# Optimization experiments

Measured on AMD Instinct MI355X. Metric: run time of the kernel, lower is better.

Reference implementation:

```python
import jax, jax.numpy as jnp
import numpy as np
from jax import lax

DIM = 512
BATCH = 8
SEQ = 2048
LR = 0.1      # learning_rate (eta)
DECAY = 0.9   # decay_rate (lambda)


def setup_inputs() -> dict:
    key = jax.random.key(0)
    ks = jax.random.split(key, 5)
    scale = DIM ** -0.5
    return {
        "x": jax.random.normal(ks[0], (BATCH, SEQ, DIM), dtype=jnp.float32),
        "Wk": jax.random.normal(ks[1], (DIM, DIM), dtype=jnp.float32) * scale,
        "bk": jnp.zeros((DIM,), dtype=jnp.float32),
        "Wv": jax.random.normal(ks[2], (DIM, DIM), dtype=jnp.float32) * scale,
        "bv": jnp.zeros((DIM,), dtype=jnp.float32),
        "Wq": jax.random.normal(ks[3], (DIM, DIM), dtype=jnp.float32) * scale,
        "bq": jnp.zeros((DIM,), dtype=jnp.float32),
        "Wo": jax.random.normal(ks[4], (DIM, DIM), dtype=jnp.float32) * scale,
        "bo": jnp.zeros((DIM,), dtype=jnp.float32),
    }


def reference(x, Wk, bk, Wv, bv, Wq, bq, Wo, bo):
    B, S, D = x.shape
    # dense projections over all tokens at once
    k = x @ Wk + bk  # (B,S,D)
    v = x @ Wv + bv
    q = x @ Wq + bq

    state0 = jnp.zeros((B, D, D), dtype=x.dtype)

    def step(state, kvq):
        k_t, v_t, q_t = kvq                                  # each (B,D)
        mem = jnp.einsum('bd,bde->be', q_t, state)           # read BEFORE update
        new_state = DECAY * state + LR * jnp.einsum('bd,be->bde', k_t, v_t)
        return new_state, mem

    # scan over time: move seq axis to front
    kT = jnp.swapaxes(k, 0, 1)  # (S,B,D)
    vT = jnp.swapaxes(v, 0, 1)
    qT = jnp.swapaxes(q, 0, 1)
    final_state, mems = lax.scan(step, state0, (kT, vT, qT))  # mems (S,B,D)

    outputs = jnp.swapaxes(mems, 0, 1)                        # (B,S,D)
    out = outputs @ Wo + bo
    return out, final_state
```

## Files before the change

### kernel.cpp

```cpp
#include <hip/hip_runtime.h>
#include <math.h>


#define DIMD 512
#define SEQL 2048
#define LRC 0.1f
#define LAM64 1.1790184577738602e-3f
#define LAM128 1.3900845237714473e-6f
#define L2LAM -0.15200309344504997f

#define KVQ_ELEMS ((size_t)16384 * 512)
#define WSLAB ((size_t)512 * 512)

typedef __attribute__((ext_vector_type(8))) short bf16x8;
typedef __attribute__((ext_vector_type(4))) float f32x4;

__device__ __forceinline__ unsigned short f2bf(float f) {
  unsigned int u = __float_as_uint(f);
  u += 0x7FFFu + ((u >> 16) & 1u);
  return (unsigned short)(u >> 16);
}

__device__ __forceinline__ void gload16(const unsigned short* g, char* l) {
  __builtin_amdgcn_global_load_lds(
      (const __attribute__((address_space(1))) unsigned int*)g,
      (__attribute__((address_space(3))) unsigned int*)l, 16, 0, 0);
}

__global__ __launch_bounds__(256) void prep(
    const float* __restrict__ x, unsigned short* __restrict__ Abf,
    const float* __restrict__ Wq, const float* __restrict__ Wk,
    const float* __restrict__ Wv, const float* __restrict__ Wo,
    unsigned short* __restrict__ T) {
  const int blk = blockIdx.x;
  if (blk < 8192) {
    const size_t idx = ((size_t)blk * 256 + threadIdx.x) * 4;
    float4 v = *(const float4*)(x + idx);
    ushort4 u;
    u.x = f2bf(v.x); u.y = f2bf(v.y); u.z = f2bf(v.z); u.w = f2bf(v.w);
    *(ushort4*)(Abf + idx) = u;
    return;
  }
  const int r2 = blk - 8192;
  const int z = r2 >> 8;
  const int rem = r2 & 255;
  const int nb = (rem & 15) * 32, kb = (rem >> 4) * 32;
  const float* W = (z == 0) ? Wq : (z == 1) ? Wk : (z == 2) ? Wv : Wo;
  unsigned short* Tz = T + (size_t)z * WSLAB;
  __shared__ float tl[32][33];
  const int r = threadIdx.x >> 5, c = threadIdx.x & 31;
#pragma unroll
  for (int i = 0; i < 4; ++i)
    tl[r + i * 8][c] = W[(size_t)(kb + r + i * 8) * 512 + nb + c];
  __syncthreads();
#pragma unroll
  for (int i = 0; i < 4; ++i)
    Tz[(size_t)(nb + r + i * 8) * 512 + kb + c] = f2bf(tl[c][r + i * 8]);
}

template <int EMODE>
__global__ __launch_bounds__(256) void mfma_gemm(
    const unsigned short* __restrict__ A, int astr,
    const unsigned short* __restrict__ T0, const unsigned short* __restrict__ T1,
    const unsigned short* __restrict__ T2, int tstr,
    const float* __restrict__ b0, const float* __restrict__ b1,
    const float* __restrict__ b2,
    float* __restrict__ Cf,
    unsigned short* __restrict__ qh, unsigned short* __restrict__ kh,
    unsigned short* __restrict__ khT, unsigned short* __restrict__ vTp,
    int nkt) {
  const int z = blockIdx.z;
  const unsigned short* T = (z == 0) ? T0 : (z == 1) ? T1 : T2;
  const float* bias = (z == 0) ? b0 : (z == 1) ? b1 : b2;

  const int m0 = blockIdx.x * 128;
  const int n0 = blockIdx.y * 128;
  const int tid = threadIdx.x;
  const int lane = tid & 63;
  const int w = tid >> 6;
  const int wm = (w & 1) * 64;
  const int wn = (w >> 1) * 64;

  __shared__ __align__(16) char smem[EMODE == 0 ? 35840 : 32768];

  f32x4 acc[4][4];
  const f32x4 zf = {0.f, 0.f, 0.f, 0.f};
#pragma unroll
  for (int i = 0; i < 4; ++i)
#pragma unroll
    for (int j = 0; j < 4; ++j) acc[i][j] = zf;

  const int lr = lane >> 3;
  const int lo3 = lane & 7;
  const int xr = lo3 ^ lr;
  const int mbase = w * 32 + lr * 2 + (xr >> 2);
  const int kel = (xr & 3) * 8;
  const unsigned short* Ag = A + (size_t)(m0 + mbase) * astr + kel;
  const unsigned short* Tg = T + (size_t)(n0 + mbase) * tstr + kel;

#define ISSUE(KT, BUF)                                                     \
  {                                                                        \
    char* ab = smem + (BUF) * 8192 + w * 2048;                             \
    char* bb_ = smem + 16384 + (BUF) * 8192 + w * 2048;                    \
    _Pragma("unroll") for (int c = 0; c < 2; ++c) {                        \
      gload16(Ag + (size_t)(c * 16) * astr + (KT) * 32, ab + c * 1024);    \
      gload16(Tg + (size_t)(c * 16) * tstr + (KT) * 32, bb_ + c * 1024);   \
    }                                                                      \
  }

  const int fr = lane & 15;
  const int fg = lane >> 4;
  const int foff = ((((fr & 1) << 6) | (fg << 4)) ^ (((fr >> 1) & 7) << 4));
  const int aline = (wm >> 1) + (fr >> 1);
  const int bline = (wn >> 1) + (fr >> 1);

  ISSUE(0, 0);
  int bb = 0;
  for (int kt = 0; kt < nkt; ++kt) {
    if (kt + 1 < nkt) {
      ISSUE(kt + 1, bb ^ 1);
      asm volatile("s_waitcnt vmcnt(4)" ::: "memory");
    } else {
      asm volatile("s_waitcnt vmcnt(0)" ::: "memory");
    }
    __builtin_amdgcn_sched_barrier(0);
    __builtin_amdgcn_s_barrier();
    const char* pa = smem + bb * 8192 + aline * 128 + foff;
    const char* pb = smem + 16384 + bb * 8192 + bline * 128 + foff;
    bf16x8 af[4], bfr[4];
#pragma unroll
    for (int mi = 0; mi < 4; ++mi) af[mi] = *(const bf16x8*)(pa + mi * 1024);
#pragma unroll
    for (int ni = 0; ni < 4; ++ni) bfr[ni] = *(const bf16x8*)(pb + ni * 1024);
#pragma unroll
    for (int mi = 0; mi < 4; ++mi)
#pragma unroll
      for (int ni = 0; ni < 4; ++ni)
        acc[mi][ni] = __builtin_amdgcn_mfma_f32_16x16x32_bf16(
            af[mi], bfr[ni], acc[mi][ni], 0, 0, 0);
    __builtin_amdgcn_s_barrier();
    __builtin_amdgcn_sched_barrier(0);
    bb ^= 1;
  }
#undef ISSUE

  const int orow = fg * 4;

  if (EMODE == 1) {
#pragma unroll
    for (int ni = 0; ni < 4; ++ni) {
      const int col = n0 + wn + ni * 16 + fr;
      const float bi = bias[col];
#pragma unroll
      for (int mi = 0; mi < 4; ++mi) {
        float* cp = Cf + (size_t)(m0 + wm + mi * 16 + orow) * 512 + col;
#pragma unroll
        for (int r = 0; r < 4; ++r) cp[(size_t)r * 512] = acc[mi][ni][r] + bi;
      }
    }
    return;
  }

  __syncthreads();
  unsigned short* cl = (unsigned short*)smem;
  const size_t batch = (size_t)(m0 >> 11);
  const int tl = m0 & 2047;

  if (z <= 1) {
#pragma unroll
    for (int ni = 0; ni < 4; ++ni) {
      const int col = wn + ni * 16 + fr;
      const float bi = bias[n0 + col];
#pragma unroll
      for (int mi = 0; mi < 4; ++mi) {
#pragma unroll
        for (int r = 0; r < 4; ++r) {
          const int row = wm + mi * 16 + orow + r;
          float v = acc[mi][ni][r] + bi;
          v *= (z == 0) ? exp2f(L2LAM * (float)(row & 63))
                        : LRC * exp2f(-L2LAM * (float)((row & 63) + 1));
          cl[row * 136 + col] = f2bf(v);
        }
      }
    }
    __syncthreads();
    {
      const int row = tid >> 1, half = tid & 1;
      unsigned short* dst = (z == 0 ? qh : kh) +
          (size_t)(m0 + row) * DIMD + n0 + half * 64;
      const unsigned short* sp = cl + row * 136 + half * 64;
#pragma unroll
      for (int j = 0; j < 8; ++j)
        *(float4*)(dst + j * 8) = *(const float4*)(sp + j * 8);
    }
  }
  if (z == 2 || (z == 1 && tl >= 1792)) {
    __syncthreads();
#pragma unroll
    for (int ni = 0; ni < 4; ++ni) {
      const int col = wn + ni * 16 + fr;
      const float bi = bias[n0 + col];
#pragma unroll
      for (int mi = 0; mi < 4; ++mi) {
#pragma unroll
        for (int r = 0; r < 4; ++r) {
          const int row = wm + mi * 16 + orow + r;
          float v = acc[mi][ni][r] + bi;
          if (z == 1) v *= LRC * exp2f(-L2LAM * (float)((row & 63) + 1));
          cl[col * 136 + row] = f2bf(v);
        }
      }
    }
    __syncthreads();
    {
      const int col = tid >> 1, half = tid & 1;
      unsigned short* dstT = (z == 1 ? khT : vTp) + batch * DIMD * SEQL +
          (size_t)(n0 + col) * SEQL + tl + half * 64;
      const unsigned short* sp = cl + col * 136 + half * 64;
#pragma unroll
      for (int j = 0; j < 8; ++j)
        *(float4*)(dstT + j * 8) = *(const float4*)(sp + j * 8);
    }
  }
}

__global__ __launch_bounds__(256) void battn(
    const unsigned short* __restrict__ qh, const unsigned short* __restrict__ kh,
    const unsigned short* __restrict__ vTp, const unsigned short* __restrict__ khT,
    unsigned short* __restrict__ mbf, float* __restrict__ fstate) {
  const int blk = blockIdx.x;
  const int tid = threadIdx.x;
  const int lane = tid & 63;
  const int w = tid >> 6;
  const int fr = lane & 15;
  const int fg = lane >> 4;

  __shared__ __align__(16) char Kl[65536];
  __shared__ __align__(16) unsigned short Pl[64 * 72];

  if (blk >= 512) {
    const int b2 = blk - 512;
    const int b = b2 & 7;
    const int slab = b2 >> 3;
    const int e0g = slab * 32;
    const int wd0 = w * 128;
    const unsigned short* kTb = khT + (size_t)b * DIMD * SEQL;
    const unsigned short* vTb = vTp + (size_t)b * DIMD * SEQL;

    f32x4 S[8][2];
    const f32x4 zf = {0.f, 0.f, 0.f, 0.f};
#pragma unroll
    for (int mi = 0; mi < 8; ++mi)
#pragma unroll
      for (int ni = 0; ni < 2; ++ni) S[mi][ni] = zf;

#pragma unroll
    for (int tb = 29; tb < 32; ++tb) {
      const int t0 = tb * 64;
#pragma unroll
      for (int ks2 = 0; ks2 < 2; ++ks2) {
        bf16x8 aK[8], bV[2];
#pragma unroll
        for (int mi = 0; mi < 8; ++mi)
          aK[mi] = *(const bf16x8*)(kTb + (size_t)(wd0 + mi * 16 + fr) * SEQL +
                                    t0 + ks2 * 32 + fg * 8);
#pragma unroll
        for (int ni = 0; ni < 2; ++ni)
          bV[ni] = *(const bf16x8*)(vTb + (size_t)(e0g + ni * 16 + fr) * SEQL +
                                    t0 + ks2 * 32 + fg * 8);
#pragma unroll
        for (int mi = 0; mi < 8; ++mi)
#pragma unroll
          for (int ni = 0; ni < 2; ++ni)
            S[mi][ni] = __builtin_amdgcn_mfma_f32_16x16x32_bf16(aK[mi], bV[ni],
                                                                S[mi][ni], 0, 0, 0);
      }
#pragma unroll
      for (int mi = 0; mi < 8; ++mi)
#pragma unroll
        for (int ni = 0; ni < 2; ++ni) {
          S[mi][ni][0] *= LAM64;
          S[mi][ni][1] *= LAM64;
          S[mi][ni][2] *= LAM64;
          S[mi][ni][3] *= LAM64;
        }
    }
    float* fs = fstate + (size_t)b * DIMD * DIMD;
#pragma unroll
    for (int mi = 0; mi < 8; ++mi)
#pragma unroll
      for (int ni = 0; ni < 2; ++ni) {
        const int e = e0g + ni * 16 + fr;
#pragma unroll
        for (int r = 0; r < 4; ++r) {
          const int d = w * 128 + mi * 16 + fg * 4 + r;
          fs[(size_t)d * DIMD + e] = S[mi][ni][r];
        }
      }
    return;
  }

  const int b = blk & 7;
  const int rest = blk >> 3;
  const int j = rest & 31;
  const int h = rest >> 5;
  const int t0 = j * 64;
  const int e0g = h * 256;
  const int wt0 = w * 16;
  const int nstartb = (j >= 2) ? 0 : (2 - j);

  const unsigned short* qb = qh + (size_t)b * SEQL * DIMD;
  const unsigned short* kb = kh + (size_t)b * SEQL * DIMD;
  const unsigned short* vTb = vTp + (size_t)b * DIMD * SEQL;
  unsigned short* mb = mbf + (size_t)b * SEQL * DIMD;

  const int selem = lane * 8;

#define STAGE(S0)                                                            \
  {                                                                          \
    _Pragma("unroll") for (int c = 0; c < 16; ++c) {                         \
      const int row = w * 16 + c;                                            \
      gload16(kb + (size_t)((S0) + row) * DIMD + (selem ^ ((row & 7) << 3)), \
              Kl + row * 1024);                                              \
    }                                                                        \
  }

  STAGE(t0 - 128 + nstartb * 64);

  bf16x8 aq[16];
  {
    const unsigned short* qrow = qb + (size_t)(t0 + wt0 + fr) * DIMD + fg * 8;
#pragma unroll
    for (int ks = 0; ks < 16; ++ks) aq[ks] = *(const bf16x8*)(qrow + ks * 32);
  }

  f32x4 mem[4][4];
  const f32x4 zf = {0.f, 0.f, 0.f, 0.f};
#pragma unroll
  for (int mi = 0; mi < 4; ++mi)
#pragma unroll
    for (int ni = 0; ni < 4; ++ni) mem[mi][ni] = zf;

  const int ew = e0g + w * 64;

  for (int sb = nstartb; sb < 3; ++sb) {
    const int s0 = t0 - 128 + sb * 64;
    __syncthreads();

    f32x4 P[4];
#pragma unroll
    for (int ni = 0; ni < 4; ++ni) P[ni] = zf;
#pragma unroll
    for (int ks = 0; ks < 16; ++ks) {
      bf16x8 bK[4];
#pragma unroll
      for (int ni = 0; ni < 4; ++ni) {
        const int row = ni * 16 + fr;
        bK[ni] = *(const bf16x8*)(Kl + row * 1024 +
                                  ((ks * 64 + fg * 16) ^ ((row & 7) << 4)));
      }
#pragma unroll
      for (int ni = 0; ni < 4; ++ni)
        P[ni] = __builtin_amdgcn_mfma_f32_16x16x32_bf16(aq[ks], bK[ni], P[ni], 0, 0, 0);
    }

#pragma unroll
    for (int ni = 0; ni < 4; ++ni) {
      const int s = ni * 16 + fr;
#pragma unroll
      for (int r = 0; r < 4; ++r) {
        const int t = wt0 + fg * 4 + r;
        float v = (sb == 0) ? P[ni][r] * LAM128
                : (sb == 1) ? P[ni][r] * LAM64
                            : ((s < t) ? P[ni][r] : 0.f);
        Pl[t * 72 + s] = f2bf(v);
      }
    }
    __syncthreads();
    if (sb + 1 < 3) STAGE(s0 + 64);

#pragma unroll
    for (int ks2 = 0; ks2 < 2; ++ks2) {
      bf16x8 ap[4];
#pragma unroll
      for (int mi = 0; mi < 4; ++mi)
        ap[mi] = *(const bf16x8*)(Pl + (mi * 16 + fr) * 72 + ks2 * 32 + fg * 8);
      const int tk = s0 + ks2 * 32 + fg * 8;
#pragma unroll
      for (int ni = 0; ni < 4; ++ni) {
        bf16x8 bV = *(const bf16x8*)(vTb + (size_t)(ew + ni * 16 + fr) * SEQL + tk);
#pragma unroll
        for (int mi = 0; mi < 4; ++mi)
          mem[mi][ni] = __builtin_amdgcn_mfma_f32_16x16x32_bf16(ap[mi], bV,
                                                               mem[mi][ni], 0, 0, 0);
      }
    }
  }
#undef STAGE

#pragma unroll
  for (int mi = 0; mi < 4; ++mi)
#pragma unroll
    for (int ni = 0; ni < 4; ++ni)
#pragma unroll
      for (int r = 0; r < 4; ++r) {
        const int t = t0 + mi * 16 + fg * 4 + r;
        mb[(size_t)t * DIMD + ew + ni * 16 + fr] = f2bf(mem[mi][ni][r]);
      }
}

extern "C" void kernel_launch(void* const* d_in, const int* in_sizes, int n_in,
                              void* d_out, int out_size, void* d_ws,
                              size_t ws_size, hipStream_t stream) {
  const float* x  = (const float*)d_in[0];
  const float* Wk = (const float*)d_in[1];
  const float* bk = (const float*)d_in[2];
  const float* Wv = (const float*)d_in[3];
  const float* bv = (const float*)d_in[4];
  const float* Wq = (const float*)d_in[5];
  const float* bq = (const float*)d_in[6];
  const float* Wo = (const float*)d_in[7];
  const float* bo = (const float*)d_in[8];

  float* outp = (float*)d_out;
  float* fstate = outp + KVQ_ELEMS;

  unsigned short* qhb = (unsigned short*)d_ws;
  unsigned short* khb = qhb + KVQ_ELEMS;
  unsigned short* khT = qhb + 2 * KVQ_ELEMS;
  unsigned short* vTp = qhb + 3 * KVQ_ELEMS;
  unsigned short* mbf = qhb + 4 * KVQ_ELEMS;
  unsigned short* WT  = qhb + 5 * KVQ_ELEMS;

  unsigned short* Abf = (unsigned short*)d_out;

  prep<<<dim3(9216), 256, 0, stream>>>(x, Abf, Wq, Wk, Wv, Wo, WT);
  mfma_gemm<0><<<dim3(128, 4, 3), 256, 0, stream>>>(
      Abf, 512, WT , WT + WSLAB , WT + 2 * WSLAB , 512,
      bq, bk, bv, nullptr, qhb, khb, khT, vTp, 16);
  battn<<<dim3(640), 256, 0, stream>>>(qhb, khb, vTp, khT, mbf, fstate);
  mfma_gemm<1><<<dim3(128, 4, 1), 256, 0, stream>>>(
      mbf, 512, WT + 3 * WSLAB, WT + 3 * WSLAB, WT + 3 * WSLAB, 512,
      bo, bo, bo, outp, nullptr, nullptr, nullptr, nullptr, 16);
}
```

Baseline: 121.2 us.

## Widen attention blocks to 512 threads covering full output width

The chunked attention kernel now launches 384 blocks of 512 threads instead of 640 blocks of 256. Each block covers all 512 output columns for one 64-token chunk, with 8 waves splitting work as 4 token groups by 2 key halves. This removes the redundant recomputation of the QK^T score tile that the old two-way column split did, and halves the per-wave K staging. The final-state blocks move to the front of the grid and split rows across 8 waves. The cost is fewer, larger blocks, which may lower occupancy and change register pressure.

```diff
diff --git a/kernel.cpp b/kernel.cpp
--- a/kernel.cpp
+++ b/kernel.cpp
@@ -224,7 +224,7 @@
   }
 }
 
-__global__ __launch_bounds__(256) void battn(
+__global__ __launch_bounds__(512) void battn(
     const unsigned short* __restrict__ qh, const unsigned short* __restrict__ kh,
     const unsigned short* __restrict__ vTp, const unsigned short* __restrict__ khT,
     unsigned short* __restrict__ mbf, float* __restrict__ fstate) {
@@ -238,19 +238,18 @@
   __shared__ __align__(16) char Kl[65536];
   __shared__ __align__(16) unsigned short Pl[64 * 72];
 
-  if (blk >= 512) {
-    const int b2 = blk - 512;
-    const int b = b2 & 7;
-    const int slab = b2 >> 3;
+  if (blk < 128) {
+    const int b = blk & 7;
+    const int slab = blk >> 3;
     const int e0g = slab * 32;
-    const int wd0 = w * 128;
+    const int wd0 = w * 64;
     const unsigned short* kTb = khT + (size_t)b * DIMD * SEQL;
     const unsigned short* vTb = vTp + (size_t)b * DIMD * SEQL;
 
-    f32x4 S[8][2];
+    f32x4 S[4][2];
     const f32x4 zf = {0.f, 0.f, 0.f, 0.f};
 #pragma unroll
-    for (int mi = 0; mi < 8; ++mi)
+    for (int mi = 0; mi < 4; ++mi)
 #pragma unroll
       for (int ni = 0; ni < 2; ++ni) S[mi][ni] = zf;
 
@@ -259,9 +258,9 @@
       const int t0 = tb * 64;
 #pragma unroll
       for (int ks2 = 0; ks2 < 2; ++ks2) {
-        bf16x8 aK[8], bV[2];
-#pragma unroll
-        for (int mi = 0; mi < 8; ++mi)
+        bf16x8 aK[4], bV[2];
+#pragma unroll
+        for (int mi = 0; mi < 4; ++mi)
           aK[mi] = *(const bf16x8*)(kTb + (size_t)(wd0 + mi * 16 + fr) * SEQL +
                                     t0 + ks2 * 32 + fg * 8);
 #pragma unroll
@@ -269,14 +268,14 @@
           bV[ni] = *(const bf16x8*)(vTb + (size_t)(e0g + ni * 16 + fr) * SEQL +
                                     t0 + ks2 * 32 + fg * 8);
 #pragma unroll
-        for (int mi = 0; mi < 8; ++mi)
+        for (int mi = 0; mi < 4; ++mi)
 #pragma unroll
           for (int ni = 0; ni < 2; ++ni)
             S[mi][ni] = __builtin_amdgcn_mfma_f32_16x16x32_bf16(aK[mi], bV[ni],
                                                                 S[mi][ni], 0, 0, 0);
       }
 #pragma unroll
-      for (int mi = 0; mi < 8; ++mi)
+      for (int mi = 0; mi < 4; ++mi)
 #pragma unroll
         for (int ni = 0; ni < 2; ++ni) {
           S[mi][ni][0] *= LAM64;
@@ -287,26 +286,26 @@
     }
     float* fs = fstate + (size_t)b * DIMD * DIMD;
 #pragma unroll
-    for (int mi = 0; mi < 8; ++mi)
+    for (int mi = 0; mi < 4; ++mi)
 #pragma unroll
       for (int ni = 0; ni < 2; ++ni) {
         const int e = e0g + ni * 16 + fr;
 #pragma unroll
         for (int r = 0; r < 4; ++r) {
-          const int d = w * 128 + mi * 16 + fg * 4 + r;
+          const int d = wd0 + mi * 16 + fg * 4 + r;
           fs[(size_t)d * DIMD + e] = S[mi][ni][r];
         }
       }
     return;
   }
 
-  const int b = blk & 7;
-  const int rest = blk >> 3;
-  const int j = rest & 31;
-  const int h = rest >> 5;
+  const int b2 = blk - 128;
+  const int b = b2 & 7;
+  const int j = b2 >> 3;
   const int t0 = j * 64;
-  const int e0g = h * 256;
-  const int wt0 = w * 16;
+  const int tg = w >> 1;
+  const int sh = w & 1;
+  const int wt0 = tg * 16;
   const int nstartb = (j >= 2) ? 0 : (2 - j);
 
   const unsigned short* qb = qh + (size_t)b * SEQL * DIMD;
@@ -318,8 +317,8 @@
 
 #define STAGE(S0)                                                            \
   {                                                                          \
-    _Pragma("unroll") for (int c = 0; c < 16; ++c) {                         \
-      const int row = w * 16 + c;                                            \
+    _Pragma("unroll") for (int c = 0; c < 8; ++c) {                          \
+      const int row = w * 8 + c;                                             \
       gload16(kb + (size_t)((S0) + row) * DIMD + (selem ^ ((row & 7) << 3)), \
               Kl + row * 1024);                                              \
     }                                                                        \
@@ -341,38 +340,38 @@
 #pragma unroll
     for (int ni = 0; ni < 4; ++ni) mem[mi][ni] = zf;
 
-  const int ew = e0g + w * 64;
+  const int ew = w * 64;
 
   for (int sb = nstartb; sb < 3; ++sb) {
     const int s0 = t0 - 128 + sb * 64;
     __syncthreads();
 
-    f32x4 P[4];
-#pragma unroll
-    for (int ni = 0; ni < 4; ++ni) P[ni] = zf;
+    f32x4 P[2];
+#pragma unroll
+    for (int nj = 0; nj < 2; ++nj) P[nj] = zf;
 #pragma unroll
     for (int ks = 0; ks < 16; ++ks) {
-      bf16x8 bK[4];
-#pragma unroll
-      for (int ni = 0; ni < 4; ++ni) {
-        const int row = ni * 16 + fr;
-        bK[ni] = *(const bf16x8*)(Kl + row * 1024 +
+      bf16x8 bK[2];
+#pragma unroll
+      for (int nj = 0; nj < 2; ++nj) {
+        const int row = sh * 32 + nj * 16 + fr;
+        bK[nj] = *(const bf16x8*)(Kl + row * 1024 +
                                   ((ks * 64 + fg * 16) ^ ((row & 7) << 4)));
       }
 #pragma unroll
-      for (int ni = 0; ni < 4; ++ni)
-        P[ni] = __builtin_amdgcn_mfma_f32_16x16x32_bf16(aq[ks], bK[ni], P[ni], 0, 0, 0);
-    }
-
-#pragma unroll
-    for (int ni = 0; ni < 4; ++ni) {
-      const int s = ni * 16 + fr;
+      for (int nj = 0; nj < 2; ++nj)
+        P[nj] = __builtin_amdgcn_mfma_f32_16x16x32_bf16(aq[ks], bK[nj], P[nj], 0, 0, 0);
+    }
+
+#pragma unroll
+    for (int nj = 0; nj < 2; ++nj) {
+      const int s = sh * 32 + nj * 16 + fr;
 #pragma unroll
       for (int r = 0; r < 4; ++r) {
         const int t = wt0 + fg * 4 + r;
-        float v = (sb == 0) ? P[ni][r] * LAM128
-                : (sb == 1) ? P[ni][r] * LAM64
-                            : ((s < t) ? P[ni][r] : 0.f);
+        float v = (sb == 0) ? P[nj][r] * LAM128
+                : (sb == 1) ? P[nj][r] * LAM64
+                            : ((s < t) ? P[nj][r] : 0.f);
         Pl[t * 72 + s] = f2bf(v);
       }
     }
@@ -438,7 +437,7 @@
   mfma_gemm<0><<<dim3(128, 4, 3), 256, 0, stream>>>(
       Abf, 512, WT , WT + WSLAB , WT + 2 * WSLAB , 512,
       bq, bk, bv, nullptr, qhb, khb, khT, vTp, 16);
-  battn<<<dim3(640), 256, 0, stream>>>(qhb, khb, vTp, khT, mbf, fstate);
+  battn<<<dim3(384), 512, 0, stream>>>(qhb, khb, vTp, khT, mbf, fstate);
   mfma_gemm<1><<<dim3(128, 4, 1), 256, 0, stream>>>(
       mbf, 512, WT + 3 * WSLAB, WT + 3 * WSLAB, WT + 3 * WSLAB, 512,
       bo, bo, bo, outp, nullptr, nullptr, nullptr, nullptr, 16);
```

After: 110.5 us. 1.1x faster.
